# Performance work log

Hardware: AMD Instinct MI355X
Metric: run time of the kernel (lower is better)

## Reference

```python
import jax, jax.numpy as jnp
import numpy as np

NOISE_SCALE = 0.1
NOISE_RATIO = 0.3
TEMPERATURE = 1.0
ADAPTIVE_FACTOR = 1.0
MAX_NOISE = 1.0


def setup_inputs() -> dict:
    key = jax.random.key(0)
    k1, k2, k3, k4 = jax.random.split(key, 4)
    B, D, C = 4096, 4096, 1000
    x = jax.random.normal(k1, (B, D), dtype=jnp.float32)
    model_output = jax.random.normal(k2, (B, C), dtype=jnp.float32)
    rand_u = jax.random.uniform(k3, (B, D), dtype=jnp.float32)
    noise_std = jax.random.normal(k4, (B, D), dtype=jnp.float32)
    return {"x": x, "model_output": model_output, "rand_u": rand_u, "noise_std": noise_std}


def reference(x, model_output, rand_u, noise_std):
    # per-sample confidence = max softmax prob of temperature-scaled logits
    probs = jax.nn.softmax(model_output / TEMPERATURE, axis=1)          # [B, C]
    confidence = jnp.max(probs, axis=1)                                  # [B]
    # adaptive per-sample noise scale, clamped at MAX_NOISE
    scales = jnp.minimum(NOISE_SCALE * (1.0 + ADAPTIVE_FACTOR * confidence), MAX_NOISE)  # [B]
    noise = noise_std * scales[:, None]                                  # [B, D]
    mask = rand_u < NOISE_RATIO                                          # [B, D] bool
    return x + jnp.where(mask, noise, jnp.zeros((), dtype=x.dtype))
```

## Files before the change

kernel.cpp:

```cpp
#include <hip/hip_runtime.h>
#include <math.h>

#define B_DIM 4096
#define D_DIM 4096
#define C_DIM 1000

__global__ __launch_bounds__(256) void adaptive_noise_kernel(
    const float* __restrict__ x,
    const float* __restrict__ model_output,
    const float* __restrict__ rand_u,
    const float* __restrict__ noise_std,
    float* __restrict__ out)
{
    const int b = blockIdx.x;
    const int t = threadIdx.x;

    float4 v;
    v.x = v.y = v.z = v.w = -INFINITY;
    const float4* mo4 = (const float4*)(model_output + (size_t)b * C_DIM);
    if (t < C_DIM / 4) v = mo4[t];

    float lm = fmaxf(fmaxf(v.x, v.y), fmaxf(v.z, v.w));
    #pragma unroll
    for (int off = 32; off > 0; off >>= 1)
        lm = fmaxf(lm, __shfl_down(lm, off, 64));

    __shared__ float red[4];
    const int wave = t >> 6;
    if ((t & 63) == 0) red[wave] = lm;
    __syncthreads();
    const float m = fmaxf(fmaxf(red[0], red[1]), fmaxf(red[2], red[3]));
    __syncthreads();

    float ls = 0.0f;
    if (t < C_DIM / 4) {
        ls = __expf(v.x - m) + __expf(v.y - m) + __expf(v.z - m) + __expf(v.w - m);
    }
    #pragma unroll
    for (int off = 32; off > 0; off >>= 1)
        ls += __shfl_down(ls, off, 64);
    if ((t & 63) == 0) red[wave] = ls;
    __syncthreads();
    const float S = (red[0] + red[1]) + (red[2] + red[3]);
    const float confidence = 1.0f / S;
    const float scale = fminf(0.1f * (1.0f + confidence), 1.0f);

    const size_t row = (size_t)b * D_DIM;
    const float4* x4 = (const float4*)(x + row);
    const float4* r4 = (const float4*)(rand_u + row);
    const float4* n4 = (const float4*)(noise_std + row);
    float4*       o4 = (float4*)(out + row);

    #pragma unroll
    for (int i = 0; i < D_DIM / 4 / 256; ++i) {
        const int idx = t + i * 256;
        float4 xv = x4[idx];
        float4 rv = r4[idx];
        float4 nv = n4[idx];
        float4 ov;
        ov.x = xv.x + (rv.x < 0.3f ? nv.x * scale : 0.0f);
        ov.y = xv.y + (rv.y < 0.3f ? nv.y * scale : 0.0f);
        ov.z = xv.z + (rv.z < 0.3f ? nv.z * scale : 0.0f);
        ov.w = xv.w + (rv.w < 0.3f ? nv.w * scale : 0.0f);
        o4[idx] = ov;
    }
}

extern "C" void kernel_launch(void* const* d_in, const int* in_sizes, int n_in,
                              void* d_out, int out_size, void* d_ws, size_t ws_size,
                              hipStream_t stream) {
    const float* x            = (const float*)d_in[0];
    const float* model_output = (const float*)d_in[1];
    const float* rand_u       = (const float*)d_in[2];
    const float* noise_std    = (const float*)d_in[3];
    float* out = (float*)d_out;

    adaptive_noise_kernel<<<B_DIM, 256, 0, stream>>>(x, model_output, rand_u, noise_std, out);
}
```

Measured before the change: 223.5 us.

## Split softmax-scale computation from noise application into two kernels

Replaces the single fused kernel with two. The first computes per-row scales using one wavefront per row and xor-shuffle reductions, with no shared memory or block barriers. The second applies the masked noise after issuing all loads up front, without waiting on a per-block reduction. The split is meant to remove the barrier-bound reduction from the bandwidth-bound elementwise path and raise memory-level parallelism, at the cost of an extra launch and a small workspace round trip.

New measurement: 227.6 us. About the same (+1.8%).

```diff
diff --git a/kernel.cpp b/kernel.cpp
--- a/kernel.cpp
+++ b/kernel.cpp
@@ -5,64 +5,76 @@
 #define D_DIM 4096
 #define C_DIM 1000
 
-__global__ __launch_bounds__(256) void adaptive_noise_kernel(
-    const float* __restrict__ x,
-    const float* __restrict__ model_output,
-    const float* __restrict__ rand_u,
-    const float* __restrict__ noise_std,
-    float* __restrict__ out)
+__global__ __launch_bounds__(256) void compute_scales(
+    const float* __restrict__ mo, float* __restrict__ scales)
 {
-    const int b = blockIdx.x;
-    const int t = threadIdx.x;
+    const int wave = threadIdx.x >> 6;
+    const int lane = threadIdx.x & 63;
+    const int row  = blockIdx.x * 4 + wave;
 
-    float4 v;
-    v.x = v.y = v.z = v.w = -INFINITY;
-    const float4* mo4 = (const float4*)(model_output + (size_t)b * C_DIM);
-    if (t < C_DIM / 4) v = mo4[t];
+    const float4* mo4 = (const float4*)(mo + (size_t)row * C_DIM);
 
-    float lm = fmaxf(fmaxf(v.x, v.y), fmaxf(v.z, v.w));
+    float4 v[4];
+    #pragma unroll
+    for (int k = 0; k < 4; ++k) {
+        const int idx = lane + k * 64;
+        if (idx < C_DIM / 4) {
+            v[k] = mo4[idx];
+        } else {
+            v[k].x = v[k].y = v[k].z = v[k].w = -INFINITY;
+        }
+    }
+
+    float m = -INFINITY;
+    #pragma unroll
+    for (int k = 0; k < 4; ++k)
+        m = fmaxf(m, fmaxf(fmaxf(v[k].x, v[k].y), fmaxf(v[k].z, v[k].w)));
     #pragma unroll
     for (int off = 32; off > 0; off >>= 1)
-        lm = fmaxf(lm, __shfl_down(lm, off, 64));
+        m = fmaxf(m, __shfl_xor(m, off, 64));
 
-    __shared__ float red[4];
-    const int wave = t >> 6;
-    if ((t & 63) == 0) red[wave] = lm;
-    __syncthreads();
-    const float m = fmaxf(fmaxf(red[0], red[1]), fmaxf(red[2], red[3]));
-    __syncthreads();
-
-    float ls = 0.0f;
-    if (t < C_DIM / 4) {
-        ls = __expf(v.x - m) + __expf(v.y - m) + __expf(v.z - m) + __expf(v.w - m);
-    }
+    float s = 0.0f;
+    #pragma unroll
+    for (int k = 0; k < 4; ++k)
+        s += __expf(v[k].x - m) + __expf(v[k].y - m)
+           + __expf(v[k].z - m) + __expf(v[k].w - m);
     #pragma unroll
     for (int off = 32; off > 0; off >>= 1)
-        ls += __shfl_down(ls, off, 64);
-    if ((t & 63) == 0) red[wave] = ls;
-    __syncthreads();
-    const float S = (red[0] + red[1]) + (red[2] + red[3]);
-    const float confidence = 1.0f / S;
-    const float scale = fminf(0.1f * (1.0f + confidence), 1.0f);
+        s += __shfl_xor(s, off, 64);
 
-    const size_t row = (size_t)b * D_DIM;
-    const float4* x4 = (const float4*)(x + row);
-    const float4* r4 = (const float4*)(rand_u + row);
-    const float4* n4 = (const float4*)(noise_std + row);
-    float4*       o4 = (float4*)(out + row);
+    if (lane == 0) {
+        const float confidence = 1.0f / s;
+        scales[row] = fminf(0.1f * (1.0f + confidence), 1.0f);
+    }
+}
+
+__global__ __launch_bounds__(256) void apply_noise(
+    const float4* __restrict__ x4,
+    const float4* __restrict__ r4,
+    const float4* __restrict__ n4,
+    const float* __restrict__ scales,
+    float4* __restrict__ o4)
+{
+    const int t = threadIdx.x;
+    const size_t base = (size_t)blockIdx.x * (D_DIM / 4);
+    const float s = scales[blockIdx.x];
+
+    float4 xv[4], rv[4], nv[4];
+    #pragma unroll
+    for (int k = 0; k < 4; ++k) xv[k] = x4[base + k * 256 + t];
+    #pragma unroll
+    for (int k = 0; k < 4; ++k) rv[k] = r4[base + k * 256 + t];
+    #pragma unroll
+    for (int k = 0; k < 4; ++k) nv[k] = n4[base + k * 256 + t];
 
     #pragma unroll
-    for (int i = 0; i < D_DIM / 4 / 256; ++i) {
-        const int idx = t + i * 256;
-        float4 xv = x4[idx];
-        float4 rv = r4[idx];
-        float4 nv = n4[idx];
+    for (int k = 0; k < 4; ++k) {
         float4 ov;
-        ov.x = xv.x + (rv.x < 0.3f ? nv.x * scale : 0.0f);
-        ov.y = xv.y + (rv.y < 0.3f ? nv.y * scale : 0.0f);
-        ov.z = xv.z + (rv.z < 0.3f ? nv.z * scale : 0.0f);
-        ov.w = xv.w + (rv.w < 0.3f ? nv.w * scale : 0.0f);
-        o4[idx] = ov;
+        ov.x = xv[k].x + (rv[k].x < 0.3f ? nv[k].x * s : 0.0f);
+        ov.y = xv[k].y + (rv[k].y < 0.3f ? nv[k].y * s : 0.0f);
+        ov.z = xv[k].z + (rv[k].z < 0.3f ? nv[k].z * s : 0.0f);
+        ov.w = xv[k].w + (rv[k].w < 0.3f ? nv[k].w * s : 0.0f);
+        o4[base + k * 256 + t] = ov;
     }
 }
 
@@ -73,7 +85,11 @@
     const float* model_output = (const float*)d_in[1];
     const float* rand_u       = (const float*)d_in[2];
     const float* noise_std    = (const float*)d_in[3];
-    float* out = (float*)d_out;
+    float* out    = (float*)d_out;
+    float* scales = (float*)d_ws;
 
-    adaptive_noise_kernel<<<B_DIM, 256, 0, stream>>>(x, model_output, rand_u, noise_std, out);
+    compute_scales<<<B_DIM / 4, 256, 0, stream>>>(model_output, scales);
+    apply_noise<<<B_DIM, 256, 0, stream>>>(
+        (const float4*)x, (const float4*)rand_u, (const float4*)noise_std,
+        scales, (float4*)out);
 }
```
